# Kernel tuning notes

Hardware: AMD Instinct MI355X
Metric: run time of the kernel (lower is better)

## Reference

```python
import jax, jax.numpy as jnp
import numpy as np

D_MODEL = 512
N_HEADS = 8
D_K = D_MODEL // N_HEADS
B = 16
S = 1024


def setup_inputs() -> dict:
    key = jax.random.key(0)
    ks = jax.random.split(key, 9)
    xavier = (2.0 / (D_MODEL + D_MODEL)) ** 0.5  # xavier_normal std for square proj
    x = jax.random.normal(ks[0], (B, S, D_MODEL), dtype=jnp.float32)
    Wq = jax.random.normal(ks[1], (D_MODEL, D_MODEL), dtype=jnp.float32) * xavier
    Wk = jax.random.normal(ks[2], (D_MODEL, D_MODEL), dtype=jnp.float32) * xavier
    Wv = jax.random.normal(ks[3], (D_MODEL, D_MODEL), dtype=jnp.float32) * xavier
    Wo = jax.random.normal(ks[4], (D_MODEL, D_MODEL), dtype=jnp.float32) * xavier
    bq = jnp.zeros((D_MODEL,), jnp.float32)
    bk = jnp.zeros((D_MODEL,), jnp.float32)
    bv = jnp.zeros((D_MODEL,), jnp.float32)
    bo = jnp.zeros((D_MODEL,), jnp.float32)
    return {"x": x, "Wq": Wq, "bq": bq, "Wk": Wk, "bk": bk,
            "Wv": Wv, "bv": bv, "Wo": Wo, "bo": bo}


def reference(x, Wq, bq, Wk, bk, Wv, bv, Wo, bo):
    # x: (B, S, D). Projections (nn.Linear applies x @ W.T + b; here W stored as (in,out)).
    b, s, _ = x.shape
    def split_heads(t):  # (B,S,D) -> (B,H,S,dk)
        return t.reshape(b, s, N_HEADS, D_K).transpose(0, 2, 1, 3)
    Q = split_heads(x @ Wq + bq)
    K = split_heads(x @ Wk + bk)
    V = split_heads(x @ Wv + bv)
    scale = 1.0 / jnp.sqrt(jnp.asarray(D_K, x.dtype))
    scores = jnp.einsum('bhqd,bhkd->bhqk', Q, K) * scale
    attn_weights = jax.nn.softmax(scores, axis=-1)
    # dropout is identity in eval mode
    ctx = jnp.einsum('bhqk,bhkd->bhqd', attn_weights, V)
    ctx = ctx.transpose(0, 2, 1, 3).reshape(b, s, D_MODEL)
    out = ctx @ Wo + bo
    return out, attn_weights
```

## Files before the change

### kernel.cpp

```cpp
#include <hip/hip_runtime.h>
#include <stdint.h>

#define D_MODELC 512
#define N_HEADSC 8
#define DKH 64
#define BATCH 16
#define SEQ 1024
#define M_TOT (BATCH*SEQ)
#define NBH (BATCH*N_HEADSC)

typedef __attribute__((ext_vector_type(8))) short short8;
typedef __attribute__((ext_vector_type(4))) float float4v;
typedef __attribute__((ext_vector_type(4))) unsigned short ushort4v;

__device__ inline unsigned short f2bf(float f) {
    unsigned u = __float_as_uint(f);
    u += 0x7FFFu + ((u >> 16) & 1u);
    return (unsigned short)(u >> 16);
}

__device__ inline void gl2lds16(const void* g, void* l) {
    __builtin_amdgcn_global_load_lds(
        (__attribute__((address_space(1))) void*)g,
        (__attribute__((address_space(3))) void*)l, 16, 0, 0);
}

__global__ void k_cvt_x(const float* __restrict__ x, unsigned short* __restrict__ xb) {
    int i = (blockIdx.x * 256 + threadIdx.x) * 4;
    float4v v = *(const float4v*)(x + i);
    ushort4v o;
    o.x = f2bf(v.x); o.y = f2bf(v.y); o.z = f2bf(v.z); o.w = f2bf(v.w);
    *(ushort4v*)(xb + i) = o;
}

__global__ void k_wt(const float* __restrict__ Wq, const float* __restrict__ Wk,
                     const float* __restrict__ Wv, const float* __restrict__ Wo,
                     unsigned short* __restrict__ Wqkvt, unsigned short* __restrict__ Wot) {
    __shared__ float tile[32][33];
    const int blk = blockIdx.x;
    const int mat = blk >> 8;
    const int t2  = blk & 255;
    const int kt = (t2 >> 4) * 32;
    const int nt = (t2 & 15) * 32;
    const float* W = mat == 0 ? Wq : mat == 1 ? Wk : mat == 2 ? Wv : Wo;
    const int tid = threadIdx.x;
    const int cx = tid & 31, ry = tid >> 5;
#pragma unroll
    for (int p = 0; p < 4; ++p) {
        int kr = ry + p * 8;
        tile[kr][cx] = W[(size_t)(kt + kr) * 512 + nt + cx];
    }
    __syncthreads();
    unsigned short* DST = (mat < 3) ? (Wqkvt + (size_t)mat * 512 * 512) : Wot;
#pragma unroll
    for (int p = 0; p < 4; ++p) {
        int nr = ry + p * 8;
        DST[(size_t)(nt + nr) * 512 + kt + cx] = f2bf(tile[cx][nr]);
    }
}

template<int MODE>
__global__ __launch_bounds__(256, 2) void k_gemm(
    const unsigned short* __restrict__ A,
    const unsigned short* __restrict__ Bt,
    const float* __restrict__ bias0,
    const float* __restrict__ bias1,
    const float* __restrict__ bias2,
    unsigned short* __restrict__ Qb,
    unsigned short* __restrict__ Kb,
    unsigned short* __restrict__ Vtb,
    float* __restrict__ Out)
{
    __shared__ __align__(16) unsigned short As[128 * 32];
    __shared__ __align__(16) unsigned short Bs[128 * 32];
    const int m0 = blockIdx.y * 128;
    const int n0 = blockIdx.x * 128;
    const int tid = threadIdx.x;
    const int w = tid >> 6, l = tid & 63;
    const int lm = l & 15, q4 = l >> 4;
    const int wm = (w >> 1) * 64, wn = (w & 1) * 64;

    float4v acc[4][4] = {};

    for (int k0 = 0; k0 < 512; k0 += 32) {
#pragma unroll
        for (int r = 0; r < 2; ++r) {
            int e = tid * 8 + r * 2048;
            int row = e >> 5, col = e & 31;
            gl2lds16(A  + (size_t)(m0 + row) * 512 + k0 + col,
                     (char*)As + w * 1024 + r * 4096);
            gl2lds16(Bt + (size_t)(n0 + row) * 512 + k0 + col,
                     (char*)Bs + w * 1024 + r * 4096);
        }
        __syncthreads();
        short8 af[4], bfr[4];
#pragma unroll
        for (int mi = 0; mi < 4; ++mi)
            af[mi] = *(const short8*)(As + (wm + mi * 16 + lm) * 32 + q4 * 8);
#pragma unroll
        for (int ni = 0; ni < 4; ++ni)
            bfr[ni] = *(const short8*)(Bs + (wn + ni * 16 + lm) * 32 + q4 * 8);
#pragma unroll
        for (int mi = 0; mi < 4; ++mi)
#pragma unroll
            for (int ni = 0; ni < 4; ++ni)
                acc[mi][ni] = __builtin_amdgcn_mfma_f32_16x16x32_bf16(
                    af[mi], bfr[ni], acc[mi][ni], 0, 0, 0);
        __syncthreads();
    }

#pragma unroll
    for (int mi = 0; mi < 4; ++mi)
#pragma unroll
        for (int ni = 0; ni < 4; ++ni)
#pragma unroll
            for (int r = 0; r < 4; ++r) {
                int m = m0 + wm + mi * 16 + q4 * 4 + r;
                int n = n0 + wn + ni * 16 + lm;
                float v = acc[mi][ni][r];
                if (MODE == 0) {
                    int which = n >> 9;
                    int nn = n & 511;
                    int h = nn >> 6, d = nn & 63;
                    int b = m >> 10, s = m & 1023;
                    size_t qkoff = (((size_t)(b * N_HEADSC + h)) * SEQ + s) * DKH + d;
                    if (which == 0) {
                        v = (v + bias0[nn]) * 0.125f;
                        Qb[qkoff] = f2bf(v);
                    } else if (which == 1) {
                        Kb[qkoff] = f2bf(v + bias1[nn]);
                    } else {
                        Vtb[(((size_t)(b * N_HEADSC + h)) * DKH + d) * SEQ + s] =
                            f2bf(v + bias2[nn]);
                    }
                } else {
                    Out[(size_t)m * 512 + n] = v + bias0[n];
                }
            }
}

__global__ __launch_bounds__(256, 2) void k_attn_pv(
    const unsigned short* __restrict__ Qb,
    const unsigned short* __restrict__ Kb,
    const unsigned short* __restrict__ Vtb,
    float* __restrict__ attn,
    unsigned short* __restrict__ ctx)
{
    __shared__ float wstat[4][32];
    __shared__ __align__(16) unsigned short Pl[4][32 * 256];
    const int blk = blockIdx.x;
    const int bh = blk >> 5;
    const int m0 = (blk & 31) * 32;
    const int tid = threadIdx.x;
    const int w = tid >> 6, l = tid & 63;
    const int lm = l & 15, q4 = l >> 4;
    const unsigned short* Qh = Qb  + (size_t)bh * SEQ * DKH;
    const unsigned short* Kh = Kb  + (size_t)bh * SEQ * DKH;
    const unsigned short* Vh = Vtb + (size_t)bh * DKH * SEQ;
    const int nw0 = w * 256;

    short8 a[2][2];
#pragma unroll
    for (int mi = 0; mi < 2; ++mi)
#pragma unroll
        for (int ks = 0; ks < 2; ++ks)
            a[mi][ks] = *(const short8*)(Qh + (size_t)(m0 + mi * 16 + lm) * 64 + ks * 32 + q4 * 8);

    float4v acc[2][16];
#pragma unroll
    for (int cg = 0; cg < 16; ++cg) {
        const unsigned short* kp = Kh + (size_t)(nw0 + cg * 16 + lm) * 64 + q4 * 8;
        short8 b0 = *(const short8*)kp;
        short8 b1 = *(const short8*)(kp + 32);
#pragma unroll
        for (int mi = 0; mi < 2; ++mi) {
            float4v z = {0.f, 0.f, 0.f, 0.f};
            z = __builtin_amdgcn_mfma_f32_16x16x32_bf16(a[mi][0], b0, z, 0, 0, 0);
            acc[mi][cg] = __builtin_amdgcn_mfma_f32_16x16x32_bf16(a[mi][1], b1, z, 0, 0, 0);
        }
    }

    float gM[2][4];
#pragma unroll
    for (int mi = 0; mi < 2; ++mi)
#pragma unroll
        for (int r = 0; r < 4; ++r) {
            float pm = -1e30f;
#pragma unroll
            for (int cg = 0; cg < 16; ++cg) pm = fmaxf(pm, acc[mi][cg][r]);
#pragma unroll
            for (int sh = 1; sh < 16; sh <<= 1) pm = fmaxf(pm, __shfl_xor(pm, sh));
            gM[mi][r] = pm;
        }
    if (lm == 0) {
#pragma unroll
        for (int mi = 0; mi < 2; ++mi)
#pragma unroll
            for (int r = 0; r < 4; ++r)
                wstat[w][mi * 16 + q4 * 4 + r] = gM[mi][r];
    }
    __syncthreads();
#pragma unroll
    for (int mi = 0; mi < 2; ++mi)
#pragma unroll
        for (int r = 0; r < 4; ++r) {
            int row = mi * 16 + q4 * 4 + r;
            gM[mi][r] = fmaxf(fmaxf(wstat[0][row], wstat[1][row]),
                              fmaxf(wstat[2][row], wstat[3][row]));
        }
    __syncthreads();

    float gS[2][4];
#pragma unroll
    for (int mi = 0; mi < 2; ++mi)
#pragma unroll
        for (int r = 0; r < 4; ++r) {
            float ps = 0.f;
#pragma unroll
            for (int cg = 0; cg < 16; ++cg) {
                float e = __expf(acc[mi][cg][r] - gM[mi][r]);
                acc[mi][cg][r] = e;
                ps += e;
            }
#pragma unroll
            for (int sh = 1; sh < 16; sh <<= 1) ps += __shfl_xor(ps, sh);
            gS[mi][r] = ps;
        }
    if (lm == 0) {
#pragma unroll
        for (int mi = 0; mi < 2; ++mi)
#pragma unroll
            for (int r = 0; r < 4; ++r)
                wstat[w][mi * 16 + q4 * 4 + r] = gS[mi][r];
    }
    __syncthreads();
    float inv[2][4];
#pragma unroll
    for (int mi = 0; mi < 2; ++mi)
#pragma unroll
        for (int r = 0; r < 4; ++r) {
            int row = mi * 16 + q4 * 4 + r;
            inv[mi][r] = 1.f / (wstat[0][row] + wstat[1][row] + wstat[2][row] + wstat[3][row]);
        }

    const size_t base = (size_t)bh * SEQ * SEQ;
    char* Pw = (char*)&Pl[w][0];
#pragma unroll
    for (int mi = 0; mi < 2; ++mi)
#pragma unroll
        for (int r = 0; r < 4; ++r) {
            const int row = mi * 16 + q4 * 4 + r;
            const int rx = (row & 7) << 4;
            const float iv = inv[mi][r];
            float* arow = attn + base + (size_t)(m0 + row) * SEQ + nw0;
#pragma unroll
            for (int cg = 0; cg < 16; ++cg) {
                float p = acc[mi][cg][r] * iv;
                arow[cg * 16 + lm] = p;
                *(unsigned short*)(Pw + row * 512 + (((cg * 16 + lm) * 2) ^ rx)) = f2bf(p);
            }
        }
    __syncthreads();

    const int rt = w & 1, dt = w >> 1;
    const int prow = rt * 16 + lm;
    const int prx  = (prow & 7) << 4;
    float4v pv[2] = {};
    for (int kc = 0; kc < 32; ++kc) {
        const int c    = kc >> 3;
        const int kloc = (kc & 7) * 32 + q4 * 8;
        const char* Pc = (const char*)&Pl[c][0];
        short8 af = *(const short8*)(Pc + prow * 512 + ((kloc * 2) ^ prx));
        const int kg = kc * 32 + q4 * 8;
#pragma unroll
        for (int ni = 0; ni < 2; ++ni) {
            short8 bfr = *(const short8*)(Vh + (size_t)(dt * 32 + ni * 16 + lm) * SEQ + kg);
            pv[ni] = __builtin_amdgcn_mfma_f32_16x16x32_bf16(af, bfr, pv[ni], 0, 0, 0);
        }
    }
    const int bb = bh >> 3, h = bh & 7;
#pragma unroll
    for (int ni = 0; ni < 2; ++ni)
#pragma unroll
        for (int r = 0; r < 4; ++r) {
            int s = m0 + rt * 16 + q4 * 4 + r;
            int d = dt * 32 + ni * 16 + lm;
            ctx[((size_t)(bb * SEQ + s)) * 512 + h * 64 + d] = f2bf(pv[ni][r]);
        }
}

extern "C" void kernel_launch(void* const* d_in, const int* in_sizes, int n_in,
                              void* d_out, int out_size, void* d_ws, size_t ws_size,
                              hipStream_t stream) {
    const float* x  = (const float*)d_in[0];
    const float* Wq = (const float*)d_in[1];
    const float* bq = (const float*)d_in[2];
    const float* Wk = (const float*)d_in[3];
    const float* bk = (const float*)d_in[4];
    const float* Wv = (const float*)d_in[5];
    const float* bv = (const float*)d_in[6];
    const float* Wo = (const float*)d_in[7];
    const float* bo = (const float*)d_in[8];

    float* out  = (float*)d_out;
    float* attn = out + (size_t)M_TOT * D_MODELC;

    char* ws = (char*)d_ws;
    unsigned short* xb    = (unsigned short*)(ws);
    unsigned short* Qb    = (unsigned short*)(ws + (size_t)(16u << 20));
    unsigned short* Kb    = (unsigned short*)(ws + (size_t)(32u << 20));
    unsigned short* Vtb   = (unsigned short*)(ws + (size_t)(48u << 20));
    unsigned short* ctxb  = (unsigned short*)(ws + (size_t)(64u << 20));
    unsigned short* Wqkvt = (unsigned short*)(ws + (size_t)(80u << 20));
    unsigned short* Wot   = (unsigned short*)(ws + (size_t)(82u << 20));

    k_cvt_x<<<8192, 256, 0, stream>>>(x, xb);
    k_wt<<<1024, 256, 0, stream>>>(Wq, Wk, Wv, Wo, Wqkvt, Wot);
    k_gemm<0><<<dim3(12, 128), 256, 0, stream>>>(xb, Wqkvt, bq, bk, bv,
                                                 Qb, Kb, Vtb, nullptr);
    k_attn_pv<<<4096, 256, 0, stream>>>(Qb, Kb, Vtb, attn, ctxb);
    k_gemm<1><<<dim3(4, 128), 256, 0, stream>>>(ctxb, Wot, bo, nullptr, nullptr,
                                                nullptr, nullptr, nullptr, out);
}
```

Measured before the change: 858.7 us.

## Swap QK operands for vectorized attn stores, remap blocks across XCDs, vectorize V store

The QK^T MFMA now takes K as the A operand and Q as B, so each lane holds four consecutive key columns for one query row. Softmax stats then reduce per row with fewer shuffles, and the fp32 attention matrix is written as 16-byte float4 stores, with the bf16 P tile written as 8-byte vectors. Block IDs in the GEMMs and the attention kernel are permuted so consecutive tiles land on the same XCD, aiming for better L2 reuse. The V-transpose epilogue writes four consecutive sequence positions as one vector store. The risk is extra index arithmetic, and the remap assumes grid sizes divisible by 8.

```diff
diff --git a/kernel.cpp b/kernel.cpp
--- a/kernel.cpp
+++ b/kernel.cpp
@@ -73,8 +73,12 @@
 {
     __shared__ __align__(16) unsigned short As[128 * 32];
     __shared__ __align__(16) unsigned short Bs[128 * 32];
-    const int m0 = blockIdx.y * 128;
-    const int n0 = blockIdx.x * 128;
+    const int NT   = (MODE == 0) ? 12 : 4;
+    const int NWG  = (MODE == 0) ? 1536 : 512;
+    int fid = blockIdx.x;
+    fid = (fid & 7) * (NWG >> 3) + (fid >> 3);
+    const int n0 = (fid % NT) * 128;
+    const int m0 = (fid / NT) * 128;
     const int tid = threadIdx.x;
     const int w = tid >> 6, l = tid & 63;
     const int lm = l & 15, q4 = l >> 4;
@@ -109,34 +113,56 @@
         __syncthreads();
     }
 
-#pragma unroll
-    for (int mi = 0; mi < 4; ++mi)
-#pragma unroll
-        for (int ni = 0; ni < 4; ++ni)
-#pragma unroll
-            for (int r = 0; r < 4; ++r) {
-                int m = m0 + wm + mi * 16 + q4 * 4 + r;
-                int n = n0 + wn + ni * 16 + lm;
-                float v = acc[mi][ni][r];
-                if (MODE == 0) {
-                    int which = n >> 9;
-                    int nn = n & 511;
+    if (MODE == 0) {
+        const int which = (n0 + wn) >> 9;
+        if (which == 2) {
+#pragma unroll
+            for (int mi = 0; mi < 4; ++mi)
+#pragma unroll
+                for (int ni = 0; ni < 4; ++ni) {
+                    int nn = (n0 + wn + ni * 16 + lm) & 511;
                     int h = nn >> 6, d = nn & 63;
-                    int b = m >> 10, s = m & 1023;
-                    size_t qkoff = (((size_t)(b * N_HEADSC + h)) * SEQ + s) * DKH + d;
-                    if (which == 0) {
-                        v = (v + bias0[nn]) * 0.125f;
-                        Qb[qkoff] = f2bf(v);
-                    } else if (which == 1) {
-                        Kb[qkoff] = f2bf(v + bias1[nn]);
-                    } else {
-                        Vtb[(((size_t)(b * N_HEADSC + h)) * DKH + d) * SEQ + s] =
-                            f2bf(v + bias2[nn]);
+                    int s0 = m0 + wm + mi * 16 + q4 * 4;
+                    int b = s0 >> 10, s = s0 & 1023;
+                    float bv2 = bias2[nn];
+                    ushort4v o;
+                    o.x = f2bf(acc[mi][ni][0] + bv2);
+                    o.y = f2bf(acc[mi][ni][1] + bv2);
+                    o.z = f2bf(acc[mi][ni][2] + bv2);
+                    o.w = f2bf(acc[mi][ni][3] + bv2);
+                    *(ushort4v*)(Vtb + (((size_t)(b * N_HEADSC + h)) * DKH + d) * SEQ + s) = o;
+                }
+        } else {
+#pragma unroll
+            for (int mi = 0; mi < 4; ++mi)
+#pragma unroll
+                for (int ni = 0; ni < 4; ++ni) {
+                    int nn = (n0 + wn + ni * 16 + lm) & 511;
+                    int h = nn >> 6, d = nn & 63;
+                    float bia = (which == 0) ? bias0[nn] : bias1[nn];
+#pragma unroll
+                    for (int r = 0; r < 4; ++r) {
+                        int m = m0 + wm + mi * 16 + q4 * 4 + r;
+                        int b = m >> 10, s = m & 1023;
+                        size_t qkoff = (((size_t)(b * N_HEADSC + h)) * SEQ + s) * DKH + d;
+                        float v = acc[mi][ni][r] + bia;
+                        if (which == 0) v *= 0.125f;
+                        ((which == 0) ? Qb : Kb)[qkoff] = f2bf(v);
                     }
-                } else {
-                    Out[(size_t)m * 512 + n] = v + bias0[n];
                 }
-            }
+        }
+    } else {
+#pragma unroll
+        for (int mi = 0; mi < 4; ++mi)
+#pragma unroll
+            for (int ni = 0; ni < 4; ++ni)
+#pragma unroll
+                for (int r = 0; r < 4; ++r) {
+                    int m = m0 + wm + mi * 16 + q4 * 4 + r;
+                    int n = n0 + wn + ni * 16 + lm;
+                    Out[(size_t)m * 512 + n] = acc[mi][ni][r] + bias0[n];
+                }
+    }
 }
 
 __global__ __launch_bounds__(256, 2) void k_attn_pv(
@@ -148,7 +174,8 @@
 {
     __shared__ float wstat[4][32];
     __shared__ __align__(16) unsigned short Pl[4][32 * 256];
-    const int blk = blockIdx.x;
+    int blk = blockIdx.x;
+    blk = (blk & 7) * 512 + (blk >> 3);
     const int bh = blk >> 5;
     const int m0 = (blk & 31) * 32;
     const int tid = threadIdx.x;
@@ -159,107 +186,98 @@
     const unsigned short* Vh = Vtb + (size_t)bh * DKH * SEQ;
     const int nw0 = w * 256;
 
-    short8 a[2][2];
+    short8 bq[2][2];
 #pragma unroll
     for (int mi = 0; mi < 2; ++mi)
 #pragma unroll
         for (int ks = 0; ks < 2; ++ks)
-            a[mi][ks] = *(const short8*)(Qh + (size_t)(m0 + mi * 16 + lm) * 64 + ks * 32 + q4 * 8);
+            bq[mi][ks] = *(const short8*)(Qh + (size_t)(m0 + mi * 16 + lm) * 64 + ks * 32 + q4 * 8);
 
     float4v acc[2][16];
 #pragma unroll
     for (int cg = 0; cg < 16; ++cg) {
         const unsigned short* kp = Kh + (size_t)(nw0 + cg * 16 + lm) * 64 + q4 * 8;
-        short8 b0 = *(const short8*)kp;
-        short8 b1 = *(const short8*)(kp + 32);
+        short8 a0 = *(const short8*)kp;
+        short8 a1 = *(const short8*)(kp + 32);
 #pragma unroll
         for (int mi = 0; mi < 2; ++mi) {
             float4v z = {0.f, 0.f, 0.f, 0.f};
-            z = __builtin_amdgcn_mfma_f32_16x16x32_bf16(a[mi][0], b0, z, 0, 0, 0);
-            acc[mi][cg] = __builtin_amdgcn_mfma_f32_16x16x32_bf16(a[mi][1], b1, z, 0, 0, 0);
-        }
-    }
-
-    float gM[2][4];
-#pragma unroll
-    for (int mi = 0; mi < 2; ++mi)
-#pragma unroll
-        for (int r = 0; r < 4; ++r) {
-            float pm = -1e30f;
-#pragma unroll
-            for (int cg = 0; cg < 16; ++cg) pm = fmaxf(pm, acc[mi][cg][r]);
-#pragma unroll
-            for (int sh = 1; sh < 16; sh <<= 1) pm = fmaxf(pm, __shfl_xor(pm, sh));
-            gM[mi][r] = pm;
-        }
-    if (lm == 0) {
-#pragma unroll
-        for (int mi = 0; mi < 2; ++mi)
-#pragma unroll
-            for (int r = 0; r < 4; ++r)
-                wstat[w][mi * 16 + q4 * 4 + r] = gM[mi][r];
-    }
-    __syncthreads();
-#pragma unroll
-    for (int mi = 0; mi < 2; ++mi)
-#pragma unroll
-        for (int r = 0; r < 4; ++r) {
-            int row = mi * 16 + q4 * 4 + r;
-            gM[mi][r] = fmaxf(fmaxf(wstat[0][row], wstat[1][row]),
-                              fmaxf(wstat[2][row], wstat[3][row]));
-        }
-    __syncthreads();
-
-    float gS[2][4];
-#pragma unroll
-    for (int mi = 0; mi < 2; ++mi)
-#pragma unroll
-        for (int r = 0; r < 4; ++r) {
-            float ps = 0.f;
-#pragma unroll
-            for (int cg = 0; cg < 16; ++cg) {
-                float e = __expf(acc[mi][cg][r] - gM[mi][r]);
+            z = __builtin_amdgcn_mfma_f32_16x16x32_bf16(a0, bq[mi][0], z, 0, 0, 0);
+            acc[mi][cg] = __builtin_amdgcn_mfma_f32_16x16x32_bf16(a1, bq[mi][1], z, 0, 0, 0);
+        }
+    }
+
+    float gM[2];
+#pragma unroll
+    for (int mi = 0; mi < 2; ++mi) {
+        float pm = -1e30f;
+#pragma unroll
+        for (int cg = 0; cg < 16; ++cg)
+#pragma unroll
+            for (int r = 0; r < 4; ++r) pm = fmaxf(pm, acc[mi][cg][r]);
+        pm = fmaxf(pm, __shfl_xor(pm, 16));
+        pm = fmaxf(pm, __shfl_xor(pm, 32));
+        gM[mi] = pm;
+    }
+    if (l < 16) {
+#pragma unroll
+        for (int mi = 0; mi < 2; ++mi) wstat[w][mi * 16 + lm] = gM[mi];
+    }
+    __syncthreads();
+#pragma unroll
+    for (int mi = 0; mi < 2; ++mi) {
+        int row = mi * 16 + lm;
+        gM[mi] = fmaxf(fmaxf(wstat[0][row], wstat[1][row]),
+                       fmaxf(wstat[2][row], wstat[3][row]));
+    }
+    __syncthreads();
+
+    float gS[2];
+#pragma unroll
+    for (int mi = 0; mi < 2; ++mi) {
+        float ps = 0.f;
+#pragma unroll
+        for (int cg = 0; cg < 16; ++cg)
+#pragma unroll
+            for (int r = 0; r < 4; ++r) {
+                float e = __expf(acc[mi][cg][r] - gM[mi]);
                 acc[mi][cg][r] = e;
                 ps += e;
             }
-#pragma unroll
-            for (int sh = 1; sh < 16; sh <<= 1) ps += __shfl_xor(ps, sh);
-            gS[mi][r] = ps;
-        }
-    if (lm == 0) {
-#pragma unroll
-        for (int mi = 0; mi < 2; ++mi)
-#pragma unroll
-            for (int r = 0; r < 4; ++r)
-                wstat[w][mi * 16 + q4 * 4 + r] = gS[mi][r];
-    }
-    __syncthreads();
-    float inv[2][4];
-#pragma unroll
-    for (int mi = 0; mi < 2; ++mi)
-#pragma unroll
-        for (int r = 0; r < 4; ++r) {
-            int row = mi * 16 + q4 * 4 + r;
-            inv[mi][r] = 1.f / (wstat[0][row] + wstat[1][row] + wstat[2][row] + wstat[3][row]);
-        }
+        ps += __shfl_xor(ps, 16);
+        ps += __shfl_xor(ps, 32);
+        gS[mi] = ps;
+    }
+    if (l < 16) {
+#pragma unroll
+        for (int mi = 0; mi < 2; ++mi) wstat[w][mi * 16 + lm] = gS[mi];
+    }
+    __syncthreads();
+    float inv[2];
+#pragma unroll
+    for (int mi = 0; mi < 2; ++mi) {
+        int row = mi * 16 + lm;
+        inv[mi] = 1.f / (wstat[0][row] + wstat[1][row] + wstat[2][row] + wstat[3][row]);
+    }
 
     const size_t base = (size_t)bh * SEQ * SEQ;
     char* Pw = (char*)&Pl[w][0];
 #pragma unroll
-    for (int mi = 0; mi < 2; ++mi)
-#pragma unroll
-        for (int r = 0; r < 4; ++r) {
-            const int row = mi * 16 + q4 * 4 + r;
-            const int rx = (row & 7) << 4;
-            const float iv = inv[mi][r];
-            float* arow = attn + base + (size_t)(m0 + row) * SEQ + nw0;
-#pragma unroll
-            for (int cg = 0; cg < 16; ++cg) {
-                float p = acc[mi][cg][r] * iv;
-                arow[cg * 16 + lm] = p;
-                *(unsigned short*)(Pw + row * 512 + (((cg * 16 + lm) * 2) ^ rx)) = f2bf(p);
-            }
-        }
+    for (int mi = 0; mi < 2; ++mi) {
+        const int row = mi * 16 + lm;
+        const int rx = (row & 7) << 4;
+        const float iv = inv[mi];
+        float* arow = attn + base + (size_t)(m0 + row) * SEQ + nw0 + q4 * 4;
+#pragma unroll
+        for (int cg = 0; cg < 16; ++cg) {
+            float4v p = acc[mi][cg] * iv;
+            *(float4v*)(arow + cg * 16) = p;
+            ushort4v pb;
+            pb.x = f2bf(p.x); pb.y = f2bf(p.y);
+            pb.z = f2bf(p.z); pb.w = f2bf(p.w);
+            *(ushort4v*)(Pw + row * 512 + ((cg * 32 + q4 * 8) ^ rx)) = pb;
+        }
+    }
     __syncthreads();
 
     const int rt = w & 1, dt = w >> 1;
@@ -316,9 +334,9 @@
 
     k_cvt_x<<<8192, 256, 0, stream>>>(x, xb);
     k_wt<<<1024, 256, 0, stream>>>(Wq, Wk, Wv, Wo, Wqkvt, Wot);
-    k_gemm<0><<<dim3(12, 128), 256, 0, stream>>>(xb, Wqkvt, bq, bk, bv,
-                                                 Qb, Kb, Vtb, nullptr);
+    k_gemm<0><<<1536, 256, 0, stream>>>(xb, Wqkvt, bq, bk, bv,
+                                        Qb, Kb, Vtb, nullptr);
     k_attn_pv<<<4096, 256, 0, stream>>>(Qb, Kb, Vtb, attn, ctxb);
-    k_gemm<1><<<dim3(4, 128), 256, 0, stream>>>(ctxb, Wot, bo, nullptr, nullptr,
-                                                nullptr, nullptr, nullptr, out);
-}
+    k_gemm<1><<<512, 256, 0, stream>>>(ctxb, Wot, bo, nullptr, nullptr,
+                                       nullptr, nullptr, nullptr, out);
+}
```

Result: faster. 839.4 us (-2.3%).
